# Optimization experiments

Hardware: AMD Instinct MI355X
Metric: run time of the kernel (lower is better)

Reference implementation:

```python
import jax, jax.numpy as jnp
import numpy as np

NUM_HEADS = 8


def _skew(x):
    # x: [b,h,l,m] with l == m. Pad last dim on the left, reshape, drop first row.
    b, h, l, m = x.shape
    x = jnp.pad(x, ((0, 0), (0, 0), (0, 0), (1, 0)))  # [b,h,l,m+1]
    return x.reshape(b, h, l + 1, m)[:, :, 1:, :]      # [b,h,l,m]


def _unskew(x):
    # Inverse skew: pad dim 2 on the left, reshape, drop first column.
    b, h, l, m = x.shape
    x = jnp.pad(x, ((0, 0), (0, 0), (1, 0), (0, 0)))  # [b,h,l+1,m]
    return x.reshape(b, h, l, m + 1)[:, :, :, 1:]      # [b,h,l,m]


def setup_inputs() -> dict:
    key = jax.random.key(0)
    B, L, D = 2, 2048, 512
    depth = D // NUM_HEADS
    ks = jax.random.split(key, 12)
    s = D ** -0.5
    inp = {
        "q": jax.random.normal(ks[0], (B, L, D), jnp.float32),
        "k": jax.random.normal(ks[1], (B, L, D), jnp.float32),
        "v": jax.random.normal(ks[2], (B, L, D), jnp.float32),
        # causal mask: 1 where attention is disallowed (future positions)
        "mask": (1.0 - jnp.tril(jnp.ones((L, L), jnp.float32)))[None, None],
        "wq": jax.random.normal(ks[3], (D, D), jnp.float32) * s,
        "bq": jnp.zeros((D,), jnp.float32),
        "wk": jax.random.normal(ks[4], (D, D), jnp.float32) * s,
        "bk": jnp.zeros((D,), jnp.float32),
        "wv": jax.random.normal(ks[5], (D, D), jnp.float32) * s,
        "bv": jnp.zeros((D,), jnp.float32),
        "wo": jax.random.normal(ks[6], (D, D), jnp.float32) * s,
        "bo": jnp.zeros((D,), jnp.float32),
        "key_rel": jax.random.normal(ks[7], (L, depth), jnp.float32) * (depth ** -0.5),
        "val_rel": jax.random.normal(ks[8], (L, depth), jnp.float32) * (depth ** -0.5),
    }
    return inp


def reference(q, k, v, mask, wq, bq, wk, bk, wv, bv, wo, bo, key_rel, val_rel):
    B, L, D = q.shape
    H = NUM_HEADS
    depth = D // H

    def split_heads(x):
        return x.reshape(B, L, H, depth).transpose(0, 2, 1, 3)  # [b,h,l,d]

    qh = split_heads(q @ wq + bq)
    kh = split_heads(k @ wk + bk)
    vh = split_heads(v @ wv + bv)

    logits = jnp.einsum('bhld,bhmd->bhlm', qh, kh)           # QK^T (no 1/sqrt(d) scale, per source)
    rel = _skew(jnp.einsum('bhld,md->bhlm', qh, key_rel))    # relative position logits
    logits = logits + rel + mask * (-1e9)
    aw = jax.nn.softmax(logits, axis=-1)                     # [b,h,l,m]

    out = jnp.einsum('bhlm,bhmd->bhld', aw, vh)
    rw = _unskew(aw)
    out = out + jnp.einsum('bhlm,md->bhld', rw, val_rel)

    out = out.transpose(0, 2, 1, 3).reshape(B, L, D)
    return out @ wo + bo, aw
```

## Files before the change

### kernel.cpp

```cpp
#include <hip/hip_runtime.h>
#include <hip/hip_bf16.h>


typedef __bf16 bf16;
typedef _Float16 f16;
typedef __attribute__((ext_vector_type(8))) __bf16 bf16x8;
typedef __attribute__((ext_vector_type(4))) float f32x4;

#define NL 2048
#define ND 512
#define NH 8
#define NM 4096

__device__ __forceinline__ f32x4 mfma16(bf16x8 a, bf16x8 b, f32x4 c) {
  return __builtin_amdgcn_mfma_f32_16x16x32_bf16(a, b, c, 0, 0, 0);
}

__device__ __forceinline__ void split_bf16(float x, bf16& h, bf16& l) {
  h = (bf16)x;
  l = (bf16)(x - (float)h);
}

__global__ __launch_bounds__(256) void k_prep(const float* __restrict__ key_rel,
                                              const float* __restrict__ val_rel,
                                              bf16* __restrict__ krr_h,
                                              bf16* __restrict__ krr_l,
                                              bf16* __restrict__ vrr_t) {
  int idx = blockIdx.x * 256 + threadIdx.x;
  int d = idx >> 6, dim = idx & 63;
  float kr = key_rel[(size_t)(NL - 1 - d) * 64 + dim];
  bf16 h, l;
  split_bf16(kr, h, l);
  krr_h[idx] = h;
  krr_l[idx] = l;
  float vr = val_rel[(size_t)(NL - 1 - d) * 64 + dim];
  vrr_t[(size_t)dim * NL + d] = (bf16)vr;
}

__global__ __launch_bounds__(256) void k_proj_qkv(
    const float* __restrict__ q, const float* __restrict__ k, const float* __restrict__ v,
    const float* __restrict__ wq, const float* __restrict__ bq,
    const float* __restrict__ wk, const float* __restrict__ bk,
    const float* __restrict__ wv, const float* __restrict__ bv,
    bf16* __restrict__ Qh, bf16* __restrict__ Ql,
    bf16* __restrict__ Kh, bf16* __restrict__ Kl, bf16* __restrict__ Vt) {
  __shared__ __align__(16) bf16 sAh[64][40], sAl[64][40];
  __shared__ __align__(16) bf16 sWh[64][40], sWl[64][40];

  int which = blockIdx.y >> 3;
  int n0 = (blockIdx.y & 7) << 6;
  int m0 = blockIdx.x << 6;
  const float* A  = which == 0 ? q  : (which == 1 ? k  : v);
  const float* Wp = which == 0 ? wq : (which == 1 ? wk : wv);
  const float* bias = which == 0 ? bq : (which == 1 ? bk : bv);

  int t = threadIdx.x;
  int wave = t >> 6, lane = t & 63, cl = lane & 15, g = lane >> 4;
  f32x4 acc[4] = {};

  for (int ks = 0; ks < 16; ++ks) {
    {
      int row = t >> 2, cb = (t & 3) << 3;
      const float* src = A + (size_t)(m0 + row) * ND + ks * 32 + cb;
      float4 v0 = *(const float4*)src;
      float4 v1 = *(const float4*)(src + 4);
      float vv[8] = {v0.x, v0.y, v0.z, v0.w, v1.x, v1.y, v1.z, v1.w};
      bf16x8 h8, l8;
#pragma unroll
      for (int e = 0; e < 8; ++e) { bf16 hh, ll; split_bf16(vv[e], hh, ll); h8[e] = hh; l8[e] = ll; }
      *(bf16x8*)&sAh[row][cb] = h8;
      *(bf16x8*)&sAl[row][cb] = l8;
    }
    {
      int kk = t >> 3, nb = (t & 7) << 3;
      const float* src = Wp + (size_t)(ks * 32 + kk) * ND + n0 + nb;
      float4 v0 = *(const float4*)src;
      float4 v1 = *(const float4*)(src + 4);
      float vv[8] = {v0.x, v0.y, v0.z, v0.w, v1.x, v1.y, v1.z, v1.w};
#pragma unroll
      for (int e = 0; e < 8; ++e) { bf16 hh, ll; split_bf16(vv[e], hh, ll); sWh[nb + e][kk] = hh; sWl[nb + e][kk] = ll; }
    }
    __syncthreads();
    bf16x8 ah = *(bf16x8*)&sAh[wave * 16 + cl][g * 8];
    bf16x8 al = *(bf16x8*)&sAl[wave * 16 + cl][g * 8];
#pragma unroll
    for (int c = 0; c < 4; ++c) {
      bf16x8 wh = *(bf16x8*)&sWh[c * 16 + cl][g * 8];
      bf16x8 wl = *(bf16x8*)&sWl[c * 16 + cl][g * 8];
      acc[c] = mfma16(ah, wh, acc[c]);
      acc[c] = mfma16(ah, wl, acc[c]);
      acc[c] = mfma16(al, wh, acc[c]);
    }
    __syncthreads();
  }

#pragma unroll
  for (int c = 0; c < 4; ++c) {
    int n = n0 + c * 16 + cl;
    int head = n >> 6, dim = n & 63;
    float bval = bias[n];
#pragma unroll
    for (int r = 0; r < 4; ++r) {
      int m = m0 + wave * 16 + g * 4 + r;
      int bb = m >> 11, lrow = m & 2047;
      float val = acc[c][r] + bval;
      if (which == 2) {
        Vt[((size_t)(bb * NH + head) * 64 + dim) * NL + lrow] = (bf16)val;
      } else {
        bf16 hh, ll;
        split_bf16(val, hh, ll);
        size_t off = ((size_t)(bb * NH + head) * NL + lrow) * 64 + dim;
        if (which == 0) { Qh[off] = hh; Ql[off] = ll; }
        else           { Kh[off] = hh; Kl[off] = ll; }
      }
    }
  }
}

__global__ __launch_bounds__(256) void k_xgemm(
    const bf16* __restrict__ Qh, const bf16* __restrict__ Ql,
    const bf16* __restrict__ krr_h, const bf16* __restrict__ krr_l,
    float* __restrict__ aw) {
  __shared__ __align__(16) bf16 sRh[64][72], sRl[64][72];
  __shared__ __align__(16) f16 sT[64][72];

  int idx = blockIdx.x;
  int qi = idx & 31;
  int bh = idx >> 5;
  if (bh >= 8) qi = 31 - qi;
  int i0 = qi << 6;

  int t = threadIdx.x;
  int wave = t >> 6, lane = t & 63, cl = lane & 15, g = lane >> 4;

  size_t qbase = ((size_t)bh * NL + (i0 + wave * 16 + cl)) * 64;
  bf16x8 qh0 = *(const bf16x8*)(Qh + qbase + g * 8);
  bf16x8 qh1 = *(const bf16x8*)(Qh + qbase + 32 + g * 8);
  bf16x8 ql0 = *(const bf16x8*)(Ql + qbase + g * 8);
  bf16x8 ql1 = *(const bf16x8*)(Ql + qbase + 32 + g * 8);

  for (int kt = 0; kt <= qi; ++kt) {
    int d0 = kt << 6;
    {
      int row = t >> 2, cb = (t & 3) << 4;
      size_t gb = (size_t)(d0 + row) * 64 + cb;
      *(uint4*)&sRh[row][cb]     = *(const uint4*)(krr_h + gb);
      *(uint4*)&sRh[row][cb + 8] = *(const uint4*)(krr_h + gb + 8);
      *(uint4*)&sRl[row][cb]     = *(const uint4*)(krr_l + gb);
      *(uint4*)&sRl[row][cb + 8] = *(const uint4*)(krr_l + gb + 8);
    }
    __syncthreads();
#pragma unroll
    for (int c = 0; c < 4; ++c) {
      int rr = c * 16 + cl;
      bf16x8 b0h = *(bf16x8*)&sRh[rr][g * 8];
      bf16x8 b0l = *(bf16x8*)&sRl[rr][g * 8];
      bf16x8 b1h = *(bf16x8*)&sRh[rr][32 + g * 8];
      bf16x8 b1l = *(bf16x8*)&sRl[rr][32 + g * 8];
      f32x4 xa = {};
      xa = mfma16(qh0, b0h, xa);
      xa = mfma16(qh1, b1h, xa);
      xa = mfma16(qh0, b0l, xa);
      xa = mfma16(qh1, b1l, xa);
      xa = mfma16(ql0, b0h, xa);
      xa = mfma16(ql1, b1h, xa);
#pragma unroll
      for (int r = 0; r < 4; ++r)
        sT[wave * 16 + g * 4 + r][c * 16 + cl] = (f16)xa[r];
    }
    __syncthreads();
#pragma unroll
    for (int it = 0; it < 16; ++it) {
      int row = it * 4 + (t >> 6), col = t & 63;
      int irow = i0 + row;
      int j = irow - d0 - col;
      if (j >= 0) {
        f16* dst = (f16*)((char*)aw + ((size_t)bh * NL + irow) * 8192);
        dst[j] = sT[row][col];
      }
    }
  }
}

__global__ __launch_bounds__(256) void k_attn(
    const bf16* __restrict__ Qh, const bf16* __restrict__ Ql,
    const bf16* __restrict__ Kh, const bf16* __restrict__ Kl,
    const bf16* __restrict__ Vt, const bf16* __restrict__ vrr_t,
    float* __restrict__ s_ws, bf16* __restrict__ O, float* __restrict__ aw) {
  __shared__ __align__(16) bf16 sKh[64][72], sKl[64][72];
  __shared__ __align__(16) bf16 sV[64][72];
  __shared__ __align__(16) f16 sXs[64][72];
  __shared__ __align__(16) bf16 sVr[64][160];
  __shared__ __align__(16) bf16 sE[4][16][72];
  __shared__ __align__(16) bf16 sEb[4][16][104];

  int idx = blockIdx.x;
  int qi = idx & 31;
  int bh = idx >> 5;
  if (bh >= 8) qi = 31 - qi;
  int i0 = qi << 6;

  int t = threadIdx.x;
  int wave = t >> 6, lane = t & 63, cl = lane & 15, g = lane >> 4;

  size_t qbase = ((size_t)bh * NL + (i0 + wave * 16 + cl)) * 64;
  bf16x8 qh0 = *(const bf16x8*)(Qh + qbase + g * 8);
  bf16x8 qh1 = *(const bf16x8*)(Qh + qbase + 32 + g * 8);
  bf16x8 ql0 = *(const bf16x8*)(Ql + qbase + g * 8);
  bf16x8 ql1 = *(const bf16x8*)(Ql + qbase + 32 + g * 8);

  f32x4 oacc[4] = {};
  float s_part[4] = {0.f, 0.f, 0.f, 0.f};

  int ntiles = qi + 1;
  for (int kt = 0; kt < ntiles; ++kt) {
    int j0 = kt << 6;
    int dmin = i0 - j0 - 63;

    {
      int row = t >> 2, cb = (t & 3) << 4;
      size_t gb = ((size_t)bh * NL + j0 + row) * 64 + cb;
      *(uint4*)&sKh[row][cb]     = *(const uint4*)(Kh + gb);
      *(uint4*)&sKh[row][cb + 8] = *(const uint4*)(Kh + gb + 8);
      *(uint4*)&sKl[row][cb]     = *(const uint4*)(Kl + gb);
      *(uint4*)&sKl[row][cb + 8] = *(const uint4*)(Kl + gb + 8);
      size_t vb = ((size_t)bh * 64 + row) * NL + j0 + cb;
      *(uint4*)&sV[row][cb]     = *(const uint4*)(Vt + vb);
      *(uint4*)&sV[row][cb + 8] = *(const uint4*)(Vt + vb + 8);
    }
    {
      int row = t >> 2, cb = (t & 3) << 4;
      const char* src = (const char*)aw + ((size_t)bh * NL + i0 + row) * 8192 + 2 * (j0 + cb);
      *(uint4*)&sXs[row][cb]     = *(const uint4*)src;
      *(uint4*)&sXs[row][cb + 8] = *(const uint4*)(src + 16);
    }
    {
      int row = t >> 2, cb0 = (t & 3) * 40;
#pragma unroll
      for (int c8 = 0; c8 < 5; ++c8) {
        int col = cb0 + c8 * 8;
        int d0 = dmin + col;
        uint4 val;
        if (d0 >= 0 && d0 + 8 <= NL) {
          val = *(const uint4*)(vrr_t + (size_t)row * NL + d0);
        } else {
          __align__(16) bf16 tmp[8];
#pragma unroll
          for (int e = 0; e < 8; ++e) {
            int d = d0 + e;
            tmp[e] = (d >= 0 && d < NL) ? vrr_t[(size_t)row * NL + d] : (bf16)0.f;
          }
          val = *(uint4*)tmp;
        }
        *(uint4*)&sVr[row][col] = val;
      }
    }
    __syncthreads();

    {
      int r = lane >> 2, cb = (lane & 3) * 24;
      uint4 z = {0, 0, 0, 0};
      *(uint4*)&sEb[wave][r][cb] = z;
      *(uint4*)&sEb[wave][r][cb + 8] = z;
      *(uint4*)&sEb[wave][r][cb + 16] = z;
    }

#pragma unroll
    for (int c = 0; c < 4; ++c) {
      int rr = c * 16 + cl;
      bf16x8 k0h = *(bf16x8*)&sKh[rr][g * 8];
      bf16x8 k0l = *(bf16x8*)&sKl[rr][g * 8];
      bf16x8 k1h = *(bf16x8*)&sKh[rr][32 + g * 8];
      bf16x8 k1l = *(bf16x8*)&sKl[rr][32 + g * 8];
      f32x4 la = {};
      la = mfma16(qh0, k0h, la);
      la = mfma16(qh1, k1h, la);
      la = mfma16(qh0, k0l, la);
      la = mfma16(qh1, k1l, la);
      la = mfma16(ql0, k0h, la);
      la = mfma16(ql1, k1h, la);
#pragma unroll
      for (int r = 0; r < 4; ++r) {
        int lr = g * 4 + r;
        int irow = i0 + wave * 16 + lr;
        int j = j0 + c * 16 + cl;
        float e = 0.f;
        if (j <= irow) {
          float X = (float)sXs[wave * 16 + lr][c * 16 + cl];
          e = __expf(la[r] + X);
        }
        s_part[r] += e;
        bf16 eb = (bf16)e;
        sE[wave][lr][c * 16 + cl] = eb;
        sEb[wave][lr][lr + 63 - c * 16 - cl] = eb;
      }
    }

#pragma unroll
    for (int dt = 0; dt < 4; ++dt) {
#pragma unroll
      for (int ks = 0; ks < 2; ++ks) {
        bf16x8 ea = *(bf16x8*)&sE[wave][cl][ks * 32 + g * 8];
        bf16x8 vb = *(bf16x8*)&sV[dt * 16 + cl][ks * 32 + g * 8];
        oacc[dt] = mfma16(ea, vb, oacc[dt]);
      }
#pragma unroll
      for (int ks = 0; ks < 3; ++ks) {
        bf16x8 ea = *(bf16x8*)&sEb[wave][cl][ks * 32 + g * 8];
        bf16x8 vb = *(bf16x8*)&sVr[dt * 16 + cl][wave * 16 + ks * 32 + g * 8];
        oacc[dt] = mfma16(ea, vb, oacc[dt]);
      }
    }

    {
      int rr = lane >> 2, cb = (lane & 3) << 4;
      char* p = (char*)aw + ((size_t)bh * NL + i0 + wave * 16 + rr) * 8192 + 4096 + 2 * (j0 + cb);
      *(uint4*)p = *(uint4*)&sE[wave][rr][cb];
      *(uint4*)(p + 16) = *(uint4*)&sE[wave][rr][cb + 8];
    }
    __syncthreads();
  }

#pragma unroll
  for (int r = 0; r < 4; ++r) {
    float vsum = s_part[r];
    vsum += __shfl_xor(vsum, 1);
    vsum += __shfl_xor(vsum, 2);
    vsum += __shfl_xor(vsum, 4);
    vsum += __shfl_xor(vsum, 8);
    s_part[r] = vsum;
  }
  if (cl == 0) {
#pragma unroll
    for (int r = 0; r < 4; ++r)
      s_ws[(size_t)bh * NL + i0 + wave * 16 + g * 4 + r] = s_part[r];
  }
  int bb = bh >> 3, hh = bh & 7;
#pragma unroll
  for (int r = 0; r < 4; ++r) {
    float inv = 1.f / s_part[r];
    int irow = i0 + wave * 16 + g * 4 + r;
    size_t obase = (size_t)(bb * NL + irow) * ND + hh * 64;
#pragma unroll
    for (int dt = 0; dt < 4; ++dt)
      O[obase + dt * 16 + cl] = (bf16)(oacc[dt][r] * inv);
  }
}

__global__ __launch_bounds__(256) void k_rescale(const float* __restrict__ s_ws,
                                                 float* __restrict__ aw) {
  int row = blockIdx.x;
  int i = row & 2047;
  int Wc = ((i >> 6) + 1) << 6;
  float inv = 1.f / s_ws[row];
  int t = threadIdx.x;
  const char* ebase = (const char*)(aw + (size_t)row * NL) + 4096;
  uint4 epack = {0, 0, 0, 0};
  if (t * 8 < Wc) epack = *(const uint4*)(ebase + 16 * t);
  __syncthreads();
  bf16x8 ev = *(bf16x8*)&epack;
  __align__(16) float vals[8];
#pragma unroll
  for (int e = 0; e < 8; ++e) {
    int j = t * 8 + e;
    vals[e] = (j <= i) ? (float)ev[e] * inv : 0.f;
  }
  float* dst = aw + (size_t)row * NL + t * 8;
  *(float4*)dst = *(float4*)&vals[0];
  *(float4*)(dst + 4) = *(float4*)&vals[4];
}

__global__ __launch_bounds__(256) void k_oproj(const bf16* __restrict__ O,
                                               const float* __restrict__ wo,
                                               const float* __restrict__ bo,
                                               float* __restrict__ out) {
  __shared__ __align__(16) bf16 sA[64][40];
  __shared__ __align__(16) bf16 sW[64][40];
  int m0 = blockIdx.x << 6, n0 = blockIdx.y << 6;
  int t = threadIdx.x;
  int wave = t >> 6, lane = t & 63, cl = lane & 15, g = lane >> 4;
  f32x4 acc[4] = {};
  for (int ks = 0; ks < 16; ++ks) {
    {
      int row = t >> 2, cb = (t & 3) << 3;
      *(uint4*)&sA[row][cb] = *(const uint4*)(O + (size_t)(m0 + row) * ND + ks * 32 + cb);
    }
    {
      int kk = t >> 3, nb = (t & 7) << 3;
      const float* src = wo + (size_t)(ks * 32 + kk) * ND + n0 + nb;
      float4 v0 = *(const float4*)src;
      float4 v1 = *(const float4*)(src + 4);
      float vv[8] = {v0.x, v0.y, v0.z, v0.w, v1.x, v1.y, v1.z, v1.w};
#pragma unroll
      for (int e = 0; e < 8; ++e) sW[nb + e][kk] = (bf16)vv[e];
    }
    __syncthreads();
    bf16x8 a = *(bf16x8*)&sA[wave * 16 + cl][g * 8];
#pragma unroll
    for (int c = 0; c < 4; ++c) {
      bf16x8 b = *(bf16x8*)&sW[c * 16 + cl][g * 8];
      acc[c] = mfma16(a, b, acc[c]);
    }
    __syncthreads();
  }
#pragma unroll
  for (int c = 0; c < 4; ++c) {
    int n = n0 + c * 16 + cl;
    float bval = bo[n];
#pragma unroll
    for (int r = 0; r < 4; ++r)
      out[(size_t)(m0 + wave * 16 + g * 4 + r) * ND + n] = acc[c][r] + bval;
  }
}

extern "C" void kernel_launch(void* const* d_in, const int* in_sizes, int n_in,
                              void* d_out, int out_size, void* d_ws, size_t ws_size,
                              hipStream_t stream) {
  const float* q  = (const float*)d_in[0];
  const float* k  = (const float*)d_in[1];
  const float* v  = (const float*)d_in[2];
  const float* wq = (const float*)d_in[4];
  const float* bq = (const float*)d_in[5];
  const float* wk = (const float*)d_in[6];
  const float* bk = (const float*)d_in[7];
  const float* wv = (const float*)d_in[8];
  const float* bv = (const float*)d_in[9];
  const float* wo = (const float*)d_in[10];
  const float* bo = (const float*)d_in[11];
  const float* key_rel = (const float*)d_in[12];
  const float* val_rel = (const float*)d_in[13];

  char* ws = (char*)d_ws;
  const size_t SZ = 4194304;
  bf16* Qh = (bf16*)(ws + 0 * SZ);
  bf16* Ql = (bf16*)(ws + 1 * SZ);
  bf16* Kh = (bf16*)(ws + 2 * SZ);
  bf16* Kl = (bf16*)(ws + 3 * SZ);
  bf16* Vt = (bf16*)(ws + 4 * SZ);
  bf16* O  = (bf16*)(ws + 5 * SZ);
  bf16* krr_h = (bf16*)(ws + 6 * SZ);
  bf16* krr_l = (bf16*)(ws + 6 * SZ + 262144);
  bf16* vrr_t = (bf16*)(ws + 6 * SZ + 2 * 262144);
  float* s_ws = (float*)(ws + 6 * SZ + 3 * 262144);

  float* out = (float*)d_out;
  float* aw = out + (size_t)NM * ND;

  k_prep<<<dim3(512), dim3(256), 0, stream>>>(key_rel, val_rel, krr_h, krr_l, vrr_t);
  k_proj_qkv<<<dim3(64, 24), dim3(256), 0, stream>>>(q, k, v, wq, bq, wk, bk, wv, bv,
                                                     Qh, Ql, Kh, Kl, Vt);
  k_xgemm<<<dim3(512), dim3(256), 0, stream>>>(Qh, Ql, krr_h, krr_l, aw);
  k_attn<<<dim3(512), dim3(256), 0, stream>>>(Qh, Ql, Kh, Kl, Vt, vrr_t, s_ws, O, aw);
  k_rescale<<<dim3(32768), dim3(256), 0, stream>>>(s_ws, aw);
  k_oproj<<<dim3(64, 8), dim3(256), 0, stream>>>(O, wo, bo, out);
}
```

Before: 606.2 us.

## Prefetch next tiles into registers and split relative-logit GEMM across two blocks

Result: faster. 555.0 us (-8.4%).

```diff
diff --git a/kernel.cpp b/kernel.cpp
--- a/kernel.cpp
+++ b/kernel.cpp
@@ -4,6 +4,7 @@
 
 typedef __bf16 bf16;
 typedef _Float16 f16;
+typedef unsigned short ushort_t;
 typedef __attribute__((ext_vector_type(8))) __bf16 bf16x8;
 typedef __attribute__((ext_vector_type(4))) float f32x4;
 
@@ -129,6 +130,10 @@
   int bh = idx >> 5;
   if (bh >= 8) qi = 31 - qi;
   int i0 = qi << 6;
+  int nt = qi + 1;
+  int kt0 = (blockIdx.y == 0) ? 0 : (nt >> 1);
+  int kt1 = (blockIdx.y == 0) ? (nt >> 1) : nt;
+  if (kt0 >= kt1) return;
 
   int t = threadIdx.x;
   int wave = t >> 6, lane = t & 63, cl = lane & 15, g = lane >> 4;
@@ -139,17 +144,25 @@
   bf16x8 ql0 = *(const bf16x8*)(Ql + qbase + g * 8);
   bf16x8 ql1 = *(const bf16x8*)(Ql + qbase + 32 + g * 8);
 
-  for (int kt = 0; kt <= qi; ++kt) {
+  int srow = t >> 2, scb = (t & 3) << 4;
+  uint4 rRh0, rRh1, rRl0, rRl1;
+  auto loadRegs = [&](int kt_) {
+    size_t gb = (size_t)((kt_ << 6) + srow) * 64 + scb;
+    rRh0 = *(const uint4*)(krr_h + gb);
+    rRh1 = *(const uint4*)(krr_h + gb + 8);
+    rRl0 = *(const uint4*)(krr_l + gb);
+    rRl1 = *(const uint4*)(krr_l + gb + 8);
+  };
+  loadRegs(kt0);
+
+  for (int kt = kt0; kt < kt1; ++kt) {
     int d0 = kt << 6;
-    {
-      int row = t >> 2, cb = (t & 3) << 4;
-      size_t gb = (size_t)(d0 + row) * 64 + cb;
-      *(uint4*)&sRh[row][cb]     = *(const uint4*)(krr_h + gb);
-      *(uint4*)&sRh[row][cb + 8] = *(const uint4*)(krr_h + gb + 8);
-      *(uint4*)&sRl[row][cb]     = *(const uint4*)(krr_l + gb);
-      *(uint4*)&sRl[row][cb + 8] = *(const uint4*)(krr_l + gb + 8);
-    }
-    __syncthreads();
+    *(uint4*)&sRh[srow][scb]     = rRh0;
+    *(uint4*)&sRh[srow][scb + 8] = rRh1;
+    *(uint4*)&sRl[srow][scb]     = rRl0;
+    *(uint4*)&sRl[srow][scb + 8] = rRl1;
+    __syncthreads();
+    if (kt + 1 < kt1) loadRegs(kt + 1);
 #pragma unroll
     for (int c = 0; c < 4; ++c) {
       int rr = c * 16 + cl;
@@ -189,8 +202,7 @@
     float* __restrict__ s_ws, bf16* __restrict__ O, float* __restrict__ aw) {
   __shared__ __align__(16) bf16 sKh[64][72], sKl[64][72];
   __shared__ __align__(16) bf16 sV[64][72];
-  __shared__ __align__(16) f16 sXs[64][72];
-  __shared__ __align__(16) bf16 sVr[64][160];
+  __shared__ __align__(16) bf16 sVr[64][168];
   __shared__ __align__(16) bf16 sE[4][16][72];
   __shared__ __align__(16) bf16 sEb[4][16][104];
 
@@ -212,51 +224,64 @@
   f32x4 oacc[4] = {};
   float s_part[4] = {0.f, 0.f, 0.f, 0.f};
 
+  int srow = t >> 2, scb = (t & 3) << 4;
+  int vcb0 = (t & 3) * 40;
+
+  uint4 rKh0, rKh1, rKl0, rKl1, rV0, rV1, rVr[5];
+  ushort_t rXs[16];
+
+  auto loadRegs = [&](int kt_) {
+    int j0_ = kt_ << 6;
+    size_t gb = ((size_t)bh * NL + j0_ + srow) * 64 + scb;
+    rKh0 = *(const uint4*)(Kh + gb);
+    rKh1 = *(const uint4*)(Kh + gb + 8);
+    rKl0 = *(const uint4*)(Kl + gb);
+    rKl1 = *(const uint4*)(Kl + gb + 8);
+    size_t vb = ((size_t)bh * 64 + srow) * NL + j0_ + scb;
+    rV0 = *(const uint4*)(Vt + vb);
+    rV1 = *(const uint4*)(Vt + vb + 8);
+    int dmin_ = i0 - j0_ - 63;
+#pragma unroll
+    for (int c8 = 0; c8 < 5; ++c8) {
+      int col = vcb0 + c8 * 8;
+      int d0v = dmin_ + col;
+      if (d0v >= 0 && d0v + 8 <= NL) {
+        rVr[c8] = *(const uint4*)(vrr_t + (size_t)srow * NL + d0v);
+      } else {
+        __align__(16) bf16 tmp[8];
+#pragma unroll
+        for (int e = 0; e < 8; ++e) {
+          int d = d0v + e;
+          tmp[e] = (d >= 0 && d < NL) ? vrr_t[(size_t)srow * NL + d] : (bf16)0.f;
+        }
+        rVr[c8] = *(uint4*)tmp;
+      }
+    }
+#pragma unroll
+    for (int r = 0; r < 4; ++r) {
+      int irow_ = i0 + wave * 16 + g * 4 + r;
+      const ushort_t* xsrow =
+          (const ushort_t*)((const char*)aw + ((size_t)bh * NL + irow_) * 8192);
+#pragma unroll
+      for (int c = 0; c < 4; ++c) rXs[r * 4 + c] = xsrow[j0_ + c * 16 + cl];
+    }
+  };
+
   int ntiles = qi + 1;
+  loadRegs(0);
+
   for (int kt = 0; kt < ntiles; ++kt) {
     int j0 = kt << 6;
-    int dmin = i0 - j0 - 63;
-
-    {
-      int row = t >> 2, cb = (t & 3) << 4;
-      size_t gb = ((size_t)bh * NL + j0 + row) * 64 + cb;
-      *(uint4*)&sKh[row][cb]     = *(const uint4*)(Kh + gb);
-      *(uint4*)&sKh[row][cb + 8] = *(const uint4*)(Kh + gb + 8);
-      *(uint4*)&sKl[row][cb]     = *(const uint4*)(Kl + gb);
-      *(uint4*)&sKl[row][cb + 8] = *(const uint4*)(Kl + gb + 8);
-      size_t vb = ((size_t)bh * 64 + row) * NL + j0 + cb;
-      *(uint4*)&sV[row][cb]     = *(const uint4*)(Vt + vb);
-      *(uint4*)&sV[row][cb + 8] = *(const uint4*)(Vt + vb + 8);
-    }
-    {
-      int row = t >> 2, cb = (t & 3) << 4;
-      const char* src = (const char*)aw + ((size_t)bh * NL + i0 + row) * 8192 + 2 * (j0 + cb);
-      *(uint4*)&sXs[row][cb]     = *(const uint4*)src;
-      *(uint4*)&sXs[row][cb + 8] = *(const uint4*)(src + 16);
-    }
-    {
-      int row = t >> 2, cb0 = (t & 3) * 40;
-#pragma unroll
-      for (int c8 = 0; c8 < 5; ++c8) {
-        int col = cb0 + c8 * 8;
-        int d0 = dmin + col;
-        uint4 val;
-        if (d0 >= 0 && d0 + 8 <= NL) {
-          val = *(const uint4*)(vrr_t + (size_t)row * NL + d0);
-        } else {
-          __align__(16) bf16 tmp[8];
-#pragma unroll
-          for (int e = 0; e < 8; ++e) {
-            int d = d0 + e;
-            tmp[e] = (d >= 0 && d < NL) ? vrr_t[(size_t)row * NL + d] : (bf16)0.f;
-          }
-          val = *(uint4*)tmp;
-        }
-        *(uint4*)&sVr[row][col] = val;
-      }
-    }
-    __syncthreads();
-
+
+    *(uint4*)&sKh[srow][scb]     = rKh0;
+    *(uint4*)&sKh[srow][scb + 8] = rKh1;
+    *(uint4*)&sKl[srow][scb]     = rKl0;
+    *(uint4*)&sKl[srow][scb + 8] = rKl1;
+    *(uint4*)&sV[srow][scb]      = rV0;
+    *(uint4*)&sV[srow][scb + 8]  = rV1;
+#pragma unroll
+    for (int c8 = 0; c8 < 5; ++c8)
+      *(uint4*)&sVr[srow][vcb0 + c8 * 8] = rVr[c8];
     {
       int r = lane >> 2, cb = (lane & 3) * 24;
       uint4 z = {0, 0, 0, 0};
@@ -264,6 +289,13 @@
       *(uint4*)&sEb[wave][r][cb + 8] = z;
       *(uint4*)&sEb[wave][r][cb + 16] = z;
     }
+    ushort_t xcur[16];
+#pragma unroll
+    for (int e = 0; e < 16; ++e) xcur[e] = rXs[e];
+
+    __syncthreads();
+
+    if (kt + 1 < ntiles) loadRegs(kt + 1);
 
 #pragma unroll
     for (int c = 0; c < 4; ++c) {
@@ -286,7 +318,7 @@
         int j = j0 + c * 16 + cl;
         float e = 0.f;
         if (j <= irow) {
-          float X = (float)sXs[wave * 16 + lr][c * 16 + cl];
+          float X = (float)(*(const f16*)&xcur[r * 4 + c]);
           e = __expf(la[r] + X);
         }
         s_part[r] += e;
@@ -449,7 +481,7 @@
   k_prep<<<dim3(512), dim3(256), 0, stream>>>(key_rel, val_rel, krr_h, krr_l, vrr_t);
   k_proj_qkv<<<dim3(64, 24), dim3(256), 0, stream>>>(q, k, v, wq, bq, wk, bk, wv, bv,
                                                      Qh, Ql, Kh, Kl, Vt);
-  k_xgemm<<<dim3(512), dim3(256), 0, stream>>>(Qh, Ql, krr_h, krr_l, aw);
+  k_xgemm<<<dim3(512, 2), dim3(256), 0, stream>>>(Qh, Ql, krr_h, krr_l, aw);
   k_attn<<<dim3(512), dim3(256), 0, stream>>>(Qh, Ql, Kh, Kl, Vt, vrr_t, s_ws, O, aw);
   k_rescale<<<dim3(32768), dim3(256), 0, stream>>>(s_ws, aw);
   k_oproj<<<dim3(64, 8), dim3(256), 0, stream>>>(O, wo, bo, out);
```

## Split key tiles across two blocks, drop LDS staging, combine partials

Applied to the files above, without the earlier changes.

New measurement: 881.2 us. 45.4% more time.

```diff
diff --git a/kernel.cpp b/kernel.cpp
--- a/kernel.cpp
+++ b/kernel.cpp
@@ -4,6 +4,7 @@
 
 typedef __bf16 bf16;
 typedef _Float16 f16;
+typedef unsigned short ushort_t;
 typedef __attribute__((ext_vector_type(8))) __bf16 bf16x8;
 typedef __attribute__((ext_vector_type(4))) float f32x4;
 
@@ -121,14 +122,18 @@
     const bf16* __restrict__ Qh, const bf16* __restrict__ Ql,
     const bf16* __restrict__ krr_h, const bf16* __restrict__ krr_l,
     float* __restrict__ aw) {
-  __shared__ __align__(16) bf16 sRh[64][72], sRl[64][72];
-  __shared__ __align__(16) f16 sT[64][72];
+  __shared__ __align__(16) f16 sT[4][16][72];
 
   int idx = blockIdx.x;
   int qi = idx & 31;
   int bh = idx >> 5;
   if (bh >= 8) qi = 31 - qi;
   int i0 = qi << 6;
+  int nt = qi + 1;
+  int y = blockIdx.y;
+  int kt0 = (y * nt) >> 1;
+  int kt1 = ((y + 1) * nt) >> 1;
+  if (kt0 >= kt1) return;
 
   int t = threadIdx.x;
   int wave = t >> 6, lane = t & 63, cl = lane & 15, g = lane >> 4;
@@ -139,24 +144,20 @@
   bf16x8 ql0 = *(const bf16x8*)(Ql + qbase + g * 8);
   bf16x8 ql1 = *(const bf16x8*)(Ql + qbase + 32 + g * 8);
 
-  for (int kt = 0; kt <= qi; ++kt) {
+  int orow = wave * 16 + (lane >> 2);
+  int ocb = (lane & 3) << 4;
+  f16* xsrow = (f16*)((char*)aw + ((size_t)bh * NL + i0 + orow) * 8192);
+
+  for (int kt = kt0; kt < kt1; ++kt) {
     int d0 = kt << 6;
-    {
-      int row = t >> 2, cb = (t & 3) << 4;
-      size_t gb = (size_t)(d0 + row) * 64 + cb;
-      *(uint4*)&sRh[row][cb]     = *(const uint4*)(krr_h + gb);
-      *(uint4*)&sRh[row][cb + 8] = *(const uint4*)(krr_h + gb + 8);
-      *(uint4*)&sRl[row][cb]     = *(const uint4*)(krr_l + gb);
-      *(uint4*)&sRl[row][cb + 8] = *(const uint4*)(krr_l + gb + 8);
-    }
-    __syncthreads();
 #pragma unroll
     for (int c = 0; c < 4; ++c) {
       int rr = c * 16 + cl;
-      bf16x8 b0h = *(bf16x8*)&sRh[rr][g * 8];
-      bf16x8 b0l = *(bf16x8*)&sRl[rr][g * 8];
-      bf16x8 b1h = *(bf16x8*)&sRh[rr][32 + g * 8];
-      bf16x8 b1l = *(bf16x8*)&sRl[rr][32 + g * 8];
+      size_t kb = (size_t)(d0 + rr) * 64 + g * 8;
+      bf16x8 b0h = *(const bf16x8*)(krr_h + kb);
+      bf16x8 b0l = *(const bf16x8*)(krr_l + kb);
+      bf16x8 b1h = *(const bf16x8*)(krr_h + kb + 32);
+      bf16x8 b1l = *(const bf16x8*)(krr_l + kb + 32);
       f32x4 xa = {};
       xa = mfma16(qh0, b0h, xa);
       xa = mfma16(qh1, b1h, xa);
@@ -166,31 +167,24 @@
       xa = mfma16(ql1, b1h, xa);
 #pragma unroll
       for (int r = 0; r < 4; ++r)
-        sT[wave * 16 + g * 4 + r][c * 16 + cl] = (f16)xa[r];
-    }
-    __syncthreads();
-#pragma unroll
-    for (int it = 0; it < 16; ++it) {
-      int row = it * 4 + (t >> 6), col = t & 63;
-      int irow = i0 + row;
-      int j = irow - d0 - col;
-      if (j >= 0) {
-        f16* dst = (f16*)((char*)aw + ((size_t)bh * NL + irow) * 8192);
-        dst[j] = sT[row][col];
-      }
-    }
-  }
-}
-
-__global__ __launch_bounds__(256) void k_attn(
+        sT[wave][g * 4 + r][63 - (c * 16 + cl)] = (f16)xa[r];
+    }
+    int jbase = (i0 + orow) - d0 - 63;
+#pragma unroll
+    for (int e = 0; e < 16; ++e) {
+      int j = jbase + ocb + e;
+      if (j >= 0) xsrow[j] = sT[wave][orow & 15][ocb + e];
+    }
+  }
+}
+
+__global__ __launch_bounds__(256, 3) void k_attn(
     const bf16* __restrict__ Qh, const bf16* __restrict__ Ql,
     const bf16* __restrict__ Kh, const bf16* __restrict__ Kl,
     const bf16* __restrict__ Vt, const bf16* __restrict__ vrr_t,
-    float* __restrict__ s_ws, bf16* __restrict__ O, float* __restrict__ aw) {
-  __shared__ __align__(16) bf16 sKh[64][72], sKl[64][72];
-  __shared__ __align__(16) bf16 sV[64][72];
-  __shared__ __align__(16) f16 sXs[64][72];
-  __shared__ __align__(16) bf16 sVr[64][160];
+    int nsplit, float* __restrict__ P0, float* __restrict__ P1,
+    float* __restrict__ s_ws0, float* __restrict__ s_ws1,
+    bf16* __restrict__ O, float* __restrict__ aw) {
   __shared__ __align__(16) bf16 sE[4][16][72];
   __shared__ __align__(16) bf16 sEb[4][16][104];
 
@@ -199,6 +193,10 @@
   int bh = idx >> 5;
   if (bh >= 8) qi = 31 - qi;
   int i0 = qi << 6;
+  int nt = qi + 1;
+  int y = blockIdx.y;
+  int kt0 = (y * nt) / nsplit;
+  int kt1 = ((y + 1) * nt) / nsplit;
 
   int t = threadIdx.x;
   int wave = t >> 6, lane = t & 63, cl = lane & 15, g = lane >> 4;
@@ -212,50 +210,15 @@
   f32x4 oacc[4] = {};
   float s_part[4] = {0.f, 0.f, 0.f, 0.f};
 
-  int ntiles = qi + 1;
-  for (int kt = 0; kt < ntiles; ++kt) {
+  const ushort_t* xsrow[4];
+#pragma unroll
+  for (int r = 0; r < 4; ++r)
+    xsrow[r] = (const ushort_t*)((const char*)aw +
+               ((size_t)bh * NL + i0 + wave * 16 + g * 4 + r) * 8192);
+
+  for (int kt = kt0; kt < kt1; ++kt) {
     int j0 = kt << 6;
     int dmin = i0 - j0 - 63;
-
-    {
-      int row = t >> 2, cb = (t & 3) << 4;
-      size_t gb = ((size_t)bh * NL + j0 + row) * 64 + cb;
-      *(uint4*)&sKh[row][cb]     = *(const uint4*)(Kh + gb);
-      *(uint4*)&sKh[row][cb + 8] = *(const uint4*)(Kh + gb + 8);
-      *(uint4*)&sKl[row][cb]     = *(const uint4*)(Kl + gb);
-      *(uint4*)&sKl[row][cb + 8] = *(const uint4*)(Kl + gb + 8);
-      size_t vb = ((size_t)bh * 64 + row) * NL + j0 + cb;
-      *(uint4*)&sV[row][cb]     = *(const uint4*)(Vt + vb);
-      *(uint4*)&sV[row][cb + 8] = *(const uint4*)(Vt + vb + 8);
-    }
-    {
-      int row = t >> 2, cb = (t & 3) << 4;
-      const char* src = (const char*)aw + ((size_t)bh * NL + i0 + row) * 8192 + 2 * (j0 + cb);
-      *(uint4*)&sXs[row][cb]     = *(const uint4*)src;
-      *(uint4*)&sXs[row][cb + 8] = *(const uint4*)(src + 16);
-    }
-    {
-      int row = t >> 2, cb0 = (t & 3) * 40;
-#pragma unroll
-      for (int c8 = 0; c8 < 5; ++c8) {
-        int col = cb0 + c8 * 8;
-        int d0 = dmin + col;
-        uint4 val;
-        if (d0 >= 0 && d0 + 8 <= NL) {
-          val = *(const uint4*)(vrr_t + (size_t)row * NL + d0);
-        } else {
-          __align__(16) bf16 tmp[8];
-#pragma unroll
-          for (int e = 0; e < 8; ++e) {
-            int d = d0 + e;
-            tmp[e] = (d >= 0 && d < NL) ? vrr_t[(size_t)row * NL + d] : (bf16)0.f;
-          }
-          val = *(uint4*)tmp;
-        }
-        *(uint4*)&sVr[row][col] = val;
-      }
-    }
-    __syncthreads();
 
     {
       int r = lane >> 2, cb = (lane & 3) * 24;
@@ -265,13 +228,20 @@
       *(uint4*)&sEb[wave][r][cb + 16] = z;
     }
 
+    ushort_t xs[16];
+#pragma unroll
+    for (int r = 0; r < 4; ++r)
+#pragma unroll
+      for (int c = 0; c < 4; ++c) xs[r * 4 + c] = xsrow[r][j0 + c * 16 + cl];
+
 #pragma unroll
     for (int c = 0; c < 4; ++c) {
       int rr = c * 16 + cl;
-      bf16x8 k0h = *(bf16x8*)&sKh[rr][g * 8];
-      bf16x8 k0l = *(bf16x8*)&sKl[rr][g * 8];
-      bf16x8 k1h = *(bf16x8*)&sKh[rr][32 + g * 8];
-      bf16x8 k1l = *(bf16x8*)&sKl[rr][32 + g * 8];
+      size_t kb = ((size_t)bh * NL + j0 + rr) * 64 + g * 8;
+      bf16x8 k0h = *(const bf16x8*)(Kh + kb);
+      bf16x8 k0l = *(const bf16x8*)(Kl + kb);
+      bf16x8 k1h = *(const bf16x8*)(Kh + kb + 32);
+      bf16x8 k1l = *(const bf16x8*)(Kl + kb + 32);
       f32x4 la = {};
       la = mfma16(qh0, k0h, la);
       la = mfma16(qh1, k1h, la);
@@ -286,7 +256,7 @@
         int j = j0 + c * 16 + cl;
         float e = 0.f;
         if (j <= irow) {
-          float X = (float)sXs[wave * 16 + lr][c * 16 + cl];
+          float X = (float)(*(const f16*)&xs[r * 4 + c]);
           e = __expf(la[r] + X);
         }
         s_part[r] += e;
@@ -298,16 +268,17 @@
 
 #pragma unroll
     for (int dt = 0; dt < 4; ++dt) {
+      int vrow = dt * 16 + cl;
 #pragma unroll
       for (int ks = 0; ks < 2; ++ks) {
         bf16x8 ea = *(bf16x8*)&sE[wave][cl][ks * 32 + g * 8];
-        bf16x8 vb = *(bf16x8*)&sV[dt * 16 + cl][ks * 32 + g * 8];
+        bf16x8 vb = *(const bf16x8*)(Vt + ((size_t)bh * 64 + vrow) * NL + j0 + ks * 32 + g * 8);
         oacc[dt] = mfma16(ea, vb, oacc[dt]);
       }
 #pragma unroll
       for (int ks = 0; ks < 3; ++ks) {
         bf16x8 ea = *(bf16x8*)&sEb[wave][cl][ks * 32 + g * 8];
-        bf16x8 vb = *(bf16x8*)&sVr[dt * 16 + cl][wave * 16 + ks * 32 + g * 8];
+        bf16x8 vb = *(const bf16x8*)(vrr_t + (size_t)vrow * NL + dmin + wave * 16 + ks * 32 + g * 8);
         oacc[dt] = mfma16(ea, vb, oacc[dt]);
       }
     }
@@ -318,7 +289,6 @@
       *(uint4*)p = *(uint4*)&sE[wave][rr][cb];
       *(uint4*)(p + 16) = *(uint4*)&sE[wave][rr][cb + 8];
     }
-    __syncthreads();
   }
 
 #pragma unroll
@@ -330,29 +300,71 @@
     vsum += __shfl_xor(vsum, 8);
     s_part[r] = vsum;
   }
-  if (cl == 0) {
-#pragma unroll
-    for (int r = 0; r < 4; ++r)
-      s_ws[(size_t)bh * NL + i0 + wave * 16 + g * 4 + r] = s_part[r];
-  }
   int bb = bh >> 3, hh = bh & 7;
-#pragma unroll
-  for (int r = 0; r < 4; ++r) {
-    float inv = 1.f / s_part[r];
-    int irow = i0 + wave * 16 + g * 4 + r;
-    size_t obase = (size_t)(bb * NL + irow) * ND + hh * 64;
-#pragma unroll
-    for (int dt = 0; dt < 4; ++dt)
-      O[obase + dt * 16 + cl] = (bf16)(oacc[dt][r] * inv);
-  }
-}
-
-__global__ __launch_bounds__(256) void k_rescale(const float* __restrict__ s_ws,
-                                                 float* __restrict__ aw) {
+  if (nsplit == 2) {
+    float* sw = (y == 0) ? s_ws0 : s_ws1;
+    float* P  = (y == 0) ? P0 : P1;
+    if (cl == 0) {
+#pragma unroll
+      for (int r = 0; r < 4; ++r)
+        sw[(size_t)bh * NL + i0 + wave * 16 + g * 4 + r] = s_part[r];
+    }
+#pragma unroll
+    for (int r = 0; r < 4; ++r) {
+      int irow = i0 + wave * 16 + g * 4 + r;
+      size_t obase = (size_t)(bb * NL + irow) * ND + hh * 64;
+#pragma unroll
+      for (int dt = 0; dt < 4; ++dt)
+        P[obase + dt * 16 + cl] = oacc[dt][r];
+    }
+  } else {
+    if (cl == 0) {
+#pragma unroll
+      for (int r = 0; r < 4; ++r)
+        s_ws0[(size_t)bh * NL + i0 + wave * 16 + g * 4 + r] = s_part[r];
+    }
+#pragma unroll
+    for (int r = 0; r < 4; ++r) {
+      float inv = 1.f / s_part[r];
+      int irow = i0 + wave * 16 + g * 4 + r;
+      size_t obase = (size_t)(bb * NL + irow) * ND + hh * 64;
+#pragma unroll
+      for (int dt = 0; dt < 4; ++dt)
+        O[obase + dt * 16 + cl] = (bf16)(oacc[dt][r] * inv);
+    }
+  }
+}
+
+__global__ __launch_bounds__(256) void k_combine(const float* __restrict__ P0,
+                                                 const float* __restrict__ P1,
+                                                 const float* __restrict__ s0,
+                                                 const float* __restrict__ s1,
+                                                 bf16* __restrict__ O) {
+  int u = blockIdx.x * 256 + threadIdx.x;
+  int n4 = u & 127, m = u >> 7;
+  int lrow = m & 2047, bb = m >> 11, hh = n4 >> 4;
+  size_t sidx = (size_t)(bb * 8 + hh) * NL + lrow;
+  float inv = 1.f / (s0[sidx] + s1[sidx]);
+  float4 a = ((const float4*)P0)[u];
+  float4 b = ((const float4*)P1)[u];
+  bf16 o0 = (bf16)((a.x + b.x) * inv);
+  bf16 o1 = (bf16)((a.y + b.y) * inv);
+  bf16 o2 = (bf16)((a.z + b.z) * inv);
+  bf16 o3 = (bf16)((a.w + b.w) * inv);
+  ushort_t pk[4];
+  pk[0] = *(ushort_t*)&o0; pk[1] = *(ushort_t*)&o1;
+  pk[2] = *(ushort_t*)&o2; pk[3] = *(ushort_t*)&o3;
+  *(uint2*)&O[(size_t)u * 4] = *(uint2*)pk;
+}
+
+__global__ __launch_bounds__(256) void k_rescale(const float* __restrict__ s0,
+                                                 const float* __restrict__ s1,
+                                                 int use2, float* __restrict__ aw) {
   int row = blockIdx.x;
   int i = row & 2047;
   int Wc = ((i >> 6) + 1) << 6;
-  float inv = 1.f / s_ws[row];
+  float s = s0[row] + (use2 ? s1[row] : 0.f);
+  float inv = 1.f / s;
   int t = threadIdx.x;
   const char* ebase = (const char*)(aw + (size_t)row * NL) + 4096;
   uint4 epack = {0, 0, 0, 0};
@@ -438,19 +450,29 @@
   bf16* Kl = (bf16*)(ws + 3 * SZ);
   bf16* Vt = (bf16*)(ws + 4 * SZ);
   bf16* O  = (bf16*)(ws + 5 * SZ);
-  bf16* krr_h = (bf16*)(ws + 6 * SZ);
-  bf16* krr_l = (bf16*)(ws + 6 * SZ + 262144);
-  bf16* vrr_t = (bf16*)(ws + 6 * SZ + 2 * 262144);
-  float* s_ws = (float*)(ws + 6 * SZ + 3 * 262144);
+  char* base6 = ws + 6 * SZ;
+  bf16* krr_h = (bf16*)(base6);
+  bf16* krr_l = (bf16*)(base6 + 262144);
+  bf16* vrr_t = (bf16*)(base6 + 2 * 262144);
+  float* s_ws0 = (float*)(base6 + 3 * 262144);
+  float* s_ws1 = (float*)(base6 + 3 * 262144 + 131072);
+  float* P1    = (float*)(base6 + 1048576);
 
   float* out = (float*)d_out;
   float* aw = out + (size_t)NM * ND;
+  float* P0 = out;
+
+  size_t need = 6 * SZ + 1048576 + (size_t)NM * ND * 4;
+  int S = (ws_size >= need) ? 2 : 1;
 
   k_prep<<<dim3(512), dim3(256), 0, stream>>>(key_rel, val_rel, krr_h, krr_l, vrr_t);
   k_proj_qkv<<<dim3(64, 24), dim3(256), 0, stream>>>(q, k, v, wq, bq, wk, bk, wv, bv,
                                                      Qh, Ql, Kh, Kl, Vt);
-  k_xgemm<<<dim3(512), dim3(256), 0, stream>>>(Qh, Ql, krr_h, krr_l, aw);
-  k_attn<<<dim3(512), dim3(256), 0, stream>>>(Qh, Ql, Kh, Kl, Vt, vrr_t, s_ws, O, aw);
-  k_rescale<<<dim3(32768), dim3(256), 0, stream>>>(s_ws, aw);
+  k_xgemm<<<dim3(512, 2), dim3(256), 0, stream>>>(Qh, Ql, krr_h, krr_l, aw);
+  k_attn<<<dim3(512, S), dim3(256), 0, stream>>>(Qh, Ql, Kh, Kl, Vt, vrr_t,
+                                                 S, P0, P1, s_ws0, s_ws1, O, aw);
+  if (S == 2)
+    k_combine<<<dim3(2048), dim3(256), 0, stream>>>(P0, P1, s_ws0, s_ws1, O);
+  k_rescale<<<dim3(32768), dim3(256), 0, stream>>>(s_ws0, s_ws1, S == 2 ? 1 : 0, aw);
   k_oproj<<<dim3(64, 8), dim3(256), 0, stream>>>(O, wo, bo, out);
 }
```
